# Kernel optimization log

Measured on AMD Instinct MI355X. Metric: run time of the kernel, lower is better.

## Reference

```python
import jax, jax.numpy as jnp
import numpy as np

B, DIN, D, C, M, NF = 64, 150528, 512, 100, 64, 256
EPS = 1e-6


def setup_inputs() -> dict:
    key = jax.random.key(0)
    ks = jax.random.split(key, 6)
    image = jax.random.normal(ks[0], (B, DIN), jnp.float32) * 0.02
    W_enc = jax.random.normal(ks[1], (DIN, D), jnp.float32) * 0.01
    text = jax.random.normal(ks[2], (C, D), jnp.float32)
    text_features = text / jnp.linalg.norm(text, axis=-1, keepdims=True)
    keys = jax.random.normal(ks[3], (C, M, D), jnp.float32)
    keys_all = keys / jnp.linalg.norm(keys, axis=-1, keepdims=True)
    indices = jax.random.randint(ks[4], (C, NF), 0, D, dtype=jnp.int32)
    return {
        "image": image,
        "W_enc": W_enc,
        "text_features": text_features,
        "keys_all": keys_all,
        "logit_scale": jnp.float32(np.log(100.0)),
        "indices": indices,
        "alpha": jnp.float32(1.0),
        "beta": jnp.float32(5.5),
        "gamma": jnp.float32(0.1),
    }


def reference(image, W_enc, text_features, keys_all, logit_scale, indices, alpha, beta, gamma):
    # image encoder (dense GEMM stand-in for clip_model.visual) + L2 normalize
    f = image @ W_enc                                    # [B, D]
    f = f / jnp.linalg.norm(f, axis=-1, keepdims=True)
    clip_logits = jnp.exp(logit_scale) * (f @ text_features.T)   # [B, C]

    # per-class feature-dim gathers (vectorized over classes)
    keys_sel = jax.vmap(lambda k, idx: k[:, idx])(keys_all, indices)      # [C, M, NF]
    text_sel = jax.vmap(lambda idx: text_features[:, idx])(indices)       # [C, C, NF]  (text_sel[c, j, f])
    img_sel = f[:, indices]                                               # [B, C, NF]

    # cache similarities: per-class [B, M] matmul, scaled by number of keys
    sims = jnp.einsum('bcf,cmf->bcm', img_sel, keys_sel) / M              # [B, C, M]

    # key logits and softmax over classes
    key_logits = jax.nn.softmax(jnp.einsum('cmf,cjf->cmj', keys_sel, text_sel), axis=-1)  # [C, M, C]

    # KL(one_hot(c) || key_logits) in log2; only the j==c term is nonzero
    p_cc = key_logits[jnp.arange(C)[:, None], jnp.arange(M)[None, :], jnp.arange(C)[:, None]]  # [C, M]
    KL = jnp.log2((1.0 + EPS) / (p_cc + EPS))                             # [C, M]
    w = jnp.exp(KL * gamma)                                               # soft_values nonzero entries

    # block-diagonal soft_values => cache_logits[b, c] = sum_m sims[b, c, m] * w[c, m]
    cache = jnp.einsum('bcm,cm->bc', sims, w)                             # [B, C]
    cache_logits = jnp.exp(-(beta - beta * cache))
    return alpha * cache_logits + clip_logits
```

## Files before the change

kernel.cpp:

```cpp
#include <hip/hip_runtime.h>

#define DIN 150528
#define DD 512
#define NC 100
#define NM 64
#define NFEAT 256
#define EPSF 1e-6f
#define KSTEPS (DIN / 32)

typedef float f32x4 __attribute__((ext_vector_type(4)));
typedef __bf16 bf16x8 __attribute__((ext_vector_type(8)));
typedef unsigned short u16x8 __attribute__((ext_vector_type(8)));

static __device__ __forceinline__ unsigned short f2bf(float x) {
  unsigned int u = __builtin_bit_cast(unsigned int, x);
  u += 0x7FFFu + ((u >> 16) & 1u);
  return (unsigned short)(u >> 16);
}
static __device__ __forceinline__ float bf2f(unsigned short h) {
  return __builtin_bit_cast(float, ((unsigned int)h) << 16);
}

__global__ __launch_bounds__(256, 1) void gemm_f(
    const float* __restrict__ image, const float* __restrict__ W,
    float* __restrict__ f_part) {
  const int tid = threadIdx.x;
  const int wv = tid >> 6;
  const int lane = tid & 63;
  const int q = lane >> 4;
  const int r16 = lane & 15;
  const int nb = wv * 128;

  f32x4 acc[4][8];
#pragma unroll
  for (int mt = 0; mt < 4; ++mt)
#pragma unroll
    for (int nt = 0; nt < 8; ++nt)
#pragma unroll
      for (int r = 0; r < 4; ++r) acc[mt][nt][r] = 0.0f;

  const int b = blockIdx.x;
  const int s0 = (b * KSTEPS) >> 8;
  const int s1 = ((b + 1) * KSTEPS) >> 8;

  for (int s = s0; s < s1; ++s) {
    const int k0 = s * 32;
    f32x4 alo[4], ahi[4];
#pragma unroll
    for (int mt = 0; mt < 4; ++mt) {
      const float* ap = image + (size_t)(mt * 16 + r16) * DIN + (k0 + q * 8);
      alo[mt] = *(const f32x4*)ap;
      ahi[mt] = *(const f32x4*)(ap + 4);
    }
    float wr[8][8];
#pragma unroll
    for (int nt = 0; nt < 8; ++nt) {
      const float* wp = W + (size_t)(k0 + q * 8) * DD + (nb + nt * 16 + r16);
#pragma unroll
      for (int j = 0; j < 8; ++j) wr[nt][j] = wp[(size_t)j * DD];
    }
    bf16x8 av[4];
#pragma unroll
    for (int mt = 0; mt < 4; ++mt) {
      u16x8 u;
      u[0] = f2bf(alo[mt][0]); u[1] = f2bf(alo[mt][1]);
      u[2] = f2bf(alo[mt][2]); u[3] = f2bf(alo[mt][3]);
      u[4] = f2bf(ahi[mt][0]); u[5] = f2bf(ahi[mt][1]);
      u[6] = f2bf(ahi[mt][2]); u[7] = f2bf(ahi[mt][3]);
      av[mt] = __builtin_bit_cast(bf16x8, u);
    }
    bf16x8 bv[8];
#pragma unroll
    for (int nt = 0; nt < 8; ++nt) {
      u16x8 u;
#pragma unroll
      for (int j = 0; j < 8; ++j) u[j] = f2bf(wr[nt][j]);
      bv[nt] = __builtin_bit_cast(bf16x8, u);
    }
#pragma unroll
    for (int mt = 0; mt < 4; ++mt)
#pragma unroll
      for (int nt = 0; nt < 8; ++nt)
        acc[mt][nt] = __builtin_amdgcn_mfma_f32_16x16x32_bf16(
            av[mt], bv[nt], acc[mt][nt], 0, 0, 0);
  }

  float* outp = f_part + (size_t)b * (NM * DD);
#pragma unroll
  for (int mt = 0; mt < 4; ++mt)
#pragma unroll
    for (int nt = 0; nt < 8; ++nt) {
      const int n = nb + nt * 16 + r16;
#pragma unroll
      for (int r = 0; r < 4; ++r) {
        const int m = mt * 16 + q * 4 + r;
        outp[m * DD + n] = acc[mt][nt][r];
      }
    }
}

__global__ __launch_bounds__(128) void reduce_f(
    const float* __restrict__ f_part, float* __restrict__ f) {
  const int m = blockIdx.x >> 2;
  const int n = (blockIdx.x & 3) * 128 + threadIdx.x;
  const float* p = f_part + (size_t)m * DD + n;
  float s = 0.0f;
#pragma unroll 16
  for (int sdx = 0; sdx < 256; ++sdx) s += p[(size_t)sdx * (NM * DD)];
  f[m * DD + n] = s;
}

__global__ void norm_f(const float* __restrict__ f, float* __restrict__ fn) {
  const int b = blockIdx.x;
  const int t = threadIdx.x;
  float s = 0.0f;
#pragma unroll
  for (int i = 0; i < 8; ++i) {
    float v = f[b * DD + t + i * 64];
    s += v * v;
  }
#pragma unroll
  for (int o = 32; o; o >>= 1) s += __shfl_xor(s, o);
  const float inv = 1.0f / sqrtf(s);
#pragma unroll
  for (int i = 0; i < 8; ++i)
    fn[b * DD + t + i * 64] = f[b * DD + t + i * 64] * inv;
}

__global__ __launch_bounds__(256) void wk_kernel(
    const float* __restrict__ text, const float* __restrict__ keys,
    const int* __restrict__ indices, const float* __restrict__ pgamma,
    float* __restrict__ kw_buf) {
  const int c = blockIdx.x;
  const int t = threadIdx.x;
  const int wv = t >> 6, lane = t & 63;
  const int q = lane >> 4, r16 = lane & 15;

  __shared__ __align__(16) unsigned short A_lds[64 * 264];
  __shared__ __align__(16) unsigned short B_lds[112 * 136];
  __shared__ __align__(16) int idx_s[256];

  idx_s[t] = indices[c * 256 + t];
  __syncthreads();

  {
    const int j = t;
    const float* kp = keys + (size_t)c * 64 * 512 + idx_s[j];
#pragma unroll 8
    for (int m = 0; m < 64; ++m) A_lds[m * 264 + j] = f2bf(kp[(size_t)m * 512]);
  }

  f32x4 acc[7];
#pragma unroll
  for (int nt = 0; nt < 7; ++nt)
#pragma unroll
    for (int r = 0; r < 4; ++r) acc[nt][r] = 0.0f;
  const int mt = wv;

  for (int kh = 0; kh < 2; ++kh) {
    __syncthreads();
    {
      const int kk = t & 127;
      const float* tp = text + idx_s[kh * 128 + kk];
      for (int n = (t >> 7); n < 112; n += 2)
        B_lds[n * 136 + kk] =
            (n < NC) ? f2bf(tp[(size_t)n * 512]) : (unsigned short)0;
    }
    __syncthreads();
#pragma unroll
    for (int ks = 0; ks < 4; ++ks) {
      bf16x8 afr = *(const bf16x8*)(A_lds + (mt * 16 + r16) * 264 + kh * 128 +
                                    ks * 32 + q * 8);
#pragma unroll
      for (int nt = 0; nt < 7; ++nt) {
        bf16x8 bfr =
            *(const bf16x8*)(B_lds + (nt * 16 + r16) * 136 + ks * 32 + q * 8);
        acc[nt] = __builtin_amdgcn_mfma_f32_16x16x32_bf16(afr, bfr, acc[nt],
                                                          0, 0, 0);
      }
    }
  }
  __syncthreads();

  float* C_lds = reinterpret_cast<float*>(B_lds);
#pragma unroll
  for (int nt = 0; nt < 7; ++nt) {
    const int j2 = nt * 16 + r16;
#pragma unroll
    for (int r = 0; r < 4; ++r) {
      const int m = mt * 16 + q * 4 + r;
      C_lds[m * 113 + j2] = acc[nt][r];
    }
  }
  __syncthreads();

  float* w_lds = reinterpret_cast<float*>(idx_s);
  if (t < 64) {
    const int m = t;
    float mx = -1e30f;
    for (int j2 = 0; j2 < NC; ++j2) mx = fmaxf(mx, C_lds[m * 113 + j2]);
    float sum = 0.0f;
    for (int j2 = 0; j2 < NC; ++j2) sum += expf(C_lds[m * 113 + j2] - mx);
    const float p = expf(C_lds[m * 113 + c] - mx) / sum;
    const float KL = log2f((1.0f + EPSF) / (p + EPSF));
    w_lds[m] = expf(KL * (*pgamma));
  }
  __syncthreads();
  {
    const int j = t;
    float kwv = 0.0f;
#pragma unroll 8
    for (int m = 0; m < 64; ++m) kwv += w_lds[m] * bf2f(A_lds[m * 264 + j]);
    kw_buf[c * 256 + j] = kwv;
  }
}

__global__ __launch_bounds__(256) void final_kernel(
    const float* __restrict__ fn, const float* __restrict__ text,
    const int* __restrict__ indices, const float* __restrict__ kw_buf,
    const float* __restrict__ pls, const float* __restrict__ palpha,
    const float* __restrict__ pbeta, float* __restrict__ out) {
  const int c = blockIdx.x;
  const int wv = threadIdx.x >> 6, lane = threadIdx.x & 63;

  int idx4[4];
  float kw4[4];
#pragma unroll
  for (int i = 0; i < 4; ++i) {
    idx4[i] = indices[c * 256 + i * 64 + lane];
    kw4[i] = kw_buf[c * 256 + i * 64 + lane];
  }
  float tc[8];
#pragma unroll
  for (int i = 0; i < 8; ++i) tc[i] = text[c * 512 + i * 64 + lane];
  const float ls = expf(*pls);
  const float alpha = *palpha, beta = *pbeta;

  for (int b = wv; b < 64; b += 4) {
    const float* fr = fn + b * DD;
    float cp = 0.0f, lp = 0.0f;
#pragma unroll
    for (int i = 0; i < 4; ++i) cp += fr[idx4[i]] * kw4[i];
#pragma unroll
    for (int i = 0; i < 8; ++i) lp += fr[i * 64 + lane] * tc[i];
#pragma unroll
    for (int o = 32; o; o >>= 1) {
      cp += __shfl_xor(cp, o);
      lp += __shfl_xor(lp, o);
    }
    if (lane == 0)
      out[b * NC + c] =
          alpha * expf(beta * (cp * (1.0f / 64.0f)) - beta) + ls * lp;
  }
}

extern "C" void kernel_launch(void* const* d_in, const int* in_sizes, int n_in,
                              void* d_out, int out_size, void* d_ws,
                              size_t ws_size, hipStream_t stream) {
  const float* image = (const float*)d_in[0];
  const float* W = (const float*)d_in[1];
  const float* text = (const float*)d_in[2];
  const float* keys = (const float*)d_in[3];
  const float* pls = (const float*)d_in[4];
  const int* idx = (const int*)d_in[5];
  const float* palpha = (const float*)d_in[6];
  const float* pbeta = (const float*)d_in[7];
  const float* pgamma = (const float*)d_in[8];
  float* out = (float*)d_out;

  char* ws = (char*)d_ws;
  float* f_part = (float*)(ws);
  float* f_buf = (float*)(ws + 33554432);
  float* fn = (float*)(ws + 33554432 + 131072);
  float* kw = (float*)(ws + 33554432 + 262144);

  gemm_f<<<256, 256, 0, stream>>>(image, W, f_part);
  reduce_f<<<256, 128, 0, stream>>>(f_part, f_buf);
  norm_f<<<64, 64, 0, stream>>>(f_buf, fn);
  wk_kernel<<<NC, 256, 0, stream>>>(text, keys, idx, pgamma, kw);
  final_kernel<<<NC, 256, 0, stream>>>(fn, text, idx, kw, pls, palpha, pbeta,
                                       out);
}
```

Baseline: 510.3 us.

## Store split-K partials in bf16 and fuse reduce/norm and wk/final kernels

The GEMM's split-K partial outputs are now written as bf16 instead of fp32, which halves the partial-buffer traffic. The reduction and L2 normalization are merged into one kernel that reads packed bf16 pairs. The per-class weight kernel and the final logits kernel are also merged so kw stays in LDS. This cuts launches and global round trips, but summing 256 bf16-rounded partials adds precision error.

```diff
diff --git a/kernel.cpp b/kernel.cpp
--- a/kernel.cpp
+++ b/kernel.cpp
@@ -9,6 +9,7 @@
 #define KSTEPS (DIN / 32)
 
 typedef float f32x4 __attribute__((ext_vector_type(4)));
+typedef float f32x2 __attribute__((ext_vector_type(2)));
 typedef __bf16 bf16x8 __attribute__((ext_vector_type(8)));
 typedef unsigned short u16x8 __attribute__((ext_vector_type(8)));
 
@@ -23,7 +24,7 @@
 
 __global__ __launch_bounds__(256, 1) void gemm_f(
     const float* __restrict__ image, const float* __restrict__ W,
-    float* __restrict__ f_part) {
+    unsigned short* __restrict__ f_part) {
   const int tid = threadIdx.x;
   const int wv = tid >> 6;
   const int lane = tid & 63;
@@ -85,7 +86,7 @@
             av[mt], bv[nt], acc[mt][nt], 0, 0, 0);
   }
 
-  float* outp = f_part + (size_t)b * (NM * DD);
+  unsigned short* outp = f_part + (size_t)b * (NM * DD);
 #pragma unroll
   for (int mt = 0; mt < 4; ++mt)
 #pragma unroll
@@ -94,43 +95,43 @@
 #pragma unroll
       for (int r = 0; r < 4; ++r) {
         const int m = mt * 16 + q * 4 + r;
-        outp[m * DD + n] = acc[mt][nt][r];
+        outp[m * DD + n] = f2bf(acc[mt][nt][r]);
       }
     }
 }
 
-__global__ __launch_bounds__(128) void reduce_f(
-    const float* __restrict__ f_part, float* __restrict__ f) {
-  const int m = blockIdx.x >> 2;
-  const int n = (blockIdx.x & 3) * 128 + threadIdx.x;
-  const float* p = f_part + (size_t)m * DD + n;
-  float s = 0.0f;
+__global__ __launch_bounds__(256) void reduce_norm(
+    const unsigned short* __restrict__ f_part, float* __restrict__ fn) {
+  const int m = blockIdx.x;
+  const int t = threadIdx.x;
+  const unsigned int* p =
+      (const unsigned int*)f_part + (size_t)m * 256 + t;
+  float s0 = 0.0f, s1 = 0.0f;
 #pragma unroll 16
-  for (int sdx = 0; sdx < 256; ++sdx) s += p[(size_t)sdx * (NM * DD)];
-  f[m * DD + n] = s;
-}
-
-__global__ void norm_f(const float* __restrict__ f, float* __restrict__ fn) {
-  const int b = blockIdx.x;
-  const int t = threadIdx.x;
-  float s = 0.0f;
-#pragma unroll
-  for (int i = 0; i < 8; ++i) {
-    float v = f[b * DD + t + i * 64];
-    s += v * v;
-  }
-#pragma unroll
-  for (int o = 32; o; o >>= 1) s += __shfl_xor(s, o);
-  const float inv = 1.0f / sqrtf(s);
-#pragma unroll
-  for (int i = 0; i < 8; ++i)
-    fn[b * DD + t + i * 64] = f[b * DD + t + i * 64] * inv;
-}
-
-__global__ __launch_bounds__(256) void wk_kernel(
+  for (int s = 0; s < 256; ++s) {
+    const unsigned int v = p[(size_t)s * (NM * DD / 2)];
+    s0 += bf2f((unsigned short)(v & 0xFFFFu));
+    s1 += bf2f((unsigned short)(v >> 16));
+  }
+  float ss = s0 * s0 + s1 * s1;
+#pragma unroll
+  for (int o = 32; o; o >>= 1) ss += __shfl_xor(ss, o);
+  __shared__ float red[4];
+  if ((t & 63) == 0) red[t >> 6] = ss;
+  __syncthreads();
+  const float inv = 1.0f / sqrtf(red[0] + red[1] + red[2] + red[3]);
+  f32x2 o2;
+  o2[0] = s0 * inv;
+  o2[1] = s1 * inv;
+  *(f32x2*)(fn + m * DD + 2 * t) = o2;
+}
+
+__global__ __launch_bounds__(256) void wk_final(
     const float* __restrict__ text, const float* __restrict__ keys,
     const int* __restrict__ indices, const float* __restrict__ pgamma,
-    float* __restrict__ kw_buf) {
+    const float* __restrict__ fn, const float* __restrict__ pls,
+    const float* __restrict__ palpha, const float* __restrict__ pbeta,
+    float* __restrict__ out) {
   const int c = blockIdx.x;
   const int t = threadIdx.x;
   const int wv = t >> 6, lane = t & 63;
@@ -206,29 +207,23 @@
     w_lds[m] = expf(KL * (*pgamma));
   }
   __syncthreads();
+
+  float* kw_lds = C_lds;
   {
     const int j = t;
     float kwv = 0.0f;
 #pragma unroll 8
     for (int m = 0; m < 64; ++m) kwv += w_lds[m] * bf2f(A_lds[m * 264 + j]);
-    kw_buf[c * 256 + j] = kwv;
-  }
-}
-
-__global__ __launch_bounds__(256) void final_kernel(
-    const float* __restrict__ fn, const float* __restrict__ text,
-    const int* __restrict__ indices, const float* __restrict__ kw_buf,
-    const float* __restrict__ pls, const float* __restrict__ palpha,
-    const float* __restrict__ pbeta, float* __restrict__ out) {
-  const int c = blockIdx.x;
-  const int wv = threadIdx.x >> 6, lane = threadIdx.x & 63;
+    kw_lds[j] = kwv;
+  }
+  __syncthreads();
 
   int idx4[4];
   float kw4[4];
 #pragma unroll
   for (int i = 0; i < 4; ++i) {
     idx4[i] = indices[c * 256 + i * 64 + lane];
-    kw4[i] = kw_buf[c * 256 + i * 64 + lane];
+    kw4[i] = kw_lds[i * 64 + lane];
   }
   float tc[8];
 #pragma unroll
@@ -269,15 +264,11 @@
   float* out = (float*)d_out;
 
   char* ws = (char*)d_ws;
-  float* f_part = (float*)(ws);
-  float* f_buf = (float*)(ws + 33554432);
-  float* fn = (float*)(ws + 33554432 + 131072);
-  float* kw = (float*)(ws + 33554432 + 262144);
+  unsigned short* f_part = (unsigned short*)ws;
+  float* fn = (float*)(ws + 16777216);
 
   gemm_f<<<256, 256, 0, stream>>>(image, W, f_part);
-  reduce_f<<<256, 128, 0, stream>>>(f_part, f_buf);
-  norm_f<<<64, 64, 0, stream>>>(f_buf, fn);
-  wk_kernel<<<NC, 256, 0, stream>>>(text, keys, idx, pgamma, kw);
-  final_kernel<<<NC, 256, 0, stream>>>(fn, text, idx, kw, pls, palpha, pbeta,
-                                       out);
-}
+  reduce_norm<<<64, 256, 0, stream>>>(f_part, fn);
+  wk_final<<<NC, 256, 0, stream>>>(text, keys, idx, pgamma, fn, pls, palpha,
+                                   pbeta, out);
+}
```

New measurement: 516.7 us. Within noise of the previous version (+1.3%).
